# Performance work log

Measured on AMD Instinct MI355X. Metric: run time of the kernel, lower is better.

Reference implementation:

```python
import jax, jax.numpy as jnp
import numpy as np

HEAD = 16
EMB = 1024
D_K = EMB // HEAD


def setup_inputs() -> dict:
    key = jax.random.key(0)
    ks = jax.random.split(key, 11)
    B, S, E = 2, 2048, EMB
    scale = 1.0 / np.sqrt(E)
    inp = {
        "query": jax.random.normal(ks[0], (B, S, E), jnp.float32),
        "key": jax.random.normal(ks[1], (B, S, E), jnp.float32),
        "value": jax.random.normal(ks[2], (B, S, E), jnp.float32),
        "Wq": jax.random.normal(ks[3], (E, E), jnp.float32) * scale,
        "bq": jnp.zeros((E,), jnp.float32),
        "Wk": jax.random.normal(ks[4], (E, E), jnp.float32) * scale,
        "bk": jnp.zeros((E,), jnp.float32),
        "Wv": jax.random.normal(ks[5], (E, E), jnp.float32) * scale,
        "bv": jnp.zeros((E,), jnp.float32),
        "Wo": jax.random.normal(ks[6], (E, E), jnp.float32) * scale,
        "bo": jnp.zeros((E,), jnp.float32),
    }
    return inp


def reference(query, key, value, Wq, bq, Wk, bk, Wv, bv, Wo, bo):
    B, S, E = query.shape
    # 3 input projections, split into heads: [B, H, S, d_k]
    def proj(x, W, b):
        return (x @ W.T + b).reshape(B, S, HEAD, D_K).transpose(0, 2, 1, 3)

    q = proj(query, Wq, bq)
    k = proj(key, Wk, bk)
    v = proj(value, Wv, bv)

    # scaled dot-product attention (full matrix, as in original)
    scores = jnp.einsum("bhqd,bhkd->bhqk", q, k) / jnp.sqrt(jnp.float32(D_K))
    attn = jax.nn.softmax(scores, axis=-1)  # dropout in eval mode = identity
    x = jnp.einsum("bhqk,bhkd->bhqd", attn, v)

    # merge heads and output projection
    x = x.transpose(0, 2, 1, 3).reshape(B, S, E)
    return x @ Wo.T + bo
```

## Files before the change

kernel.cpp:

```cpp
#include <hip/hip_runtime.h>
#include <hip/hip_bf16.h>
#include <math.h>


constexpr int Sn = 2048;
constexpr int En = 1024;
constexpr int Hn = 16;
constexpr int Dk = 64;
constexpr int Kn = 1024;
constexpr size_t WSZ = 1048576;
constexpr size_t TSZ = 4194304;

#define QSCALE 0.18033688011112042f

typedef __bf16 bf16x8 __attribute__((ext_vector_type(8)));
typedef float  f32x4  __attribute__((ext_vector_type(4)));
typedef float  f32x16 __attribute__((ext_vector_type(16)));

union U16 { uint4 u; bf16x8 v; __hip_bfloat16 h[8]; };
union U8  { uint2 u; __hip_bfloat162 h2[2]; __hip_bfloat16 h[4]; };
union U4  { unsigned u; __hip_bfloat162 h2; };

__device__ inline U16 cvt8f(const float* __restrict__ p) {
    float4 a = *(const float4*)p;
    float4 b = *(const float4*)(p + 4);
    U16 r;
    r.h[0] = __float2bfloat16(a.x); r.h[1] = __float2bfloat16(a.y);
    r.h[2] = __float2bfloat16(a.z); r.h[3] = __float2bfloat16(a.w);
    r.h[4] = __float2bfloat16(b.x); r.h[5] = __float2bfloat16(b.y);
    r.h[6] = __float2bfloat16(b.z); r.h[7] = __float2bfloat16(b.w);
    return r;
}

__device__ inline void gload16(const __hip_bfloat16* g, __hip_bfloat16* l) {
    __builtin_amdgcn_global_load_lds(
        (const __attribute__((address_space(1))) void*)g,
        (__attribute__((address_space(3))) void*)l, 16, 0, 0);
}

template<int ROWS, int NW>
__device__ inline void stage_tile(const __hip_bfloat16* __restrict__ src, int ld,
                                  __hip_bfloat16* lds, int w, int lane) {
    int l8 = lane >> 3;
    int g = (lane & 7) ^ (l8 & 7);
    #pragma unroll
    for (int j = 0; j < ROWS / (8 * NW); ++j) {
        int c = j * NW + w;
        gload16(src + (size_t)(c * 8 + l8) * ld + g * 8, lds + c * 512);
    }
}

__global__ __launch_bounds__(256)
void cvt_w(const float* __restrict__ w0, const float* __restrict__ w1,
           const float* __restrict__ w2, const float* __restrict__ w3,
           __hip_bfloat16* __restrict__ dst)
{
    int y = blockIdx.y;
    const float* src = (y == 0) ? w0 : (y == 1) ? w1 : (y == 2) ? w2 : w3;
    size_t i = ((size_t)blockIdx.x * 256 + threadIdx.x) * 8;
    U16 r = cvt8f(src + i);
    *(uint4*)&dst[(size_t)y * WSZ + i] = r.u;
}

__global__ __launch_bounds__(256)
void cvt_x3(const float* __restrict__ q, const float* __restrict__ k,
            const float* __restrict__ v, __hip_bfloat16* __restrict__ dst)
{
    int z = blockIdx.y;
    const float* src = (z == 0) ? q : (z == 1) ? k : v;
    size_t i = ((size_t)blockIdx.x * 256 + threadIdx.x) * 8;
    U16 r = cvt8f(src + i);
    *(uint4*)&dst[(size_t)z * TSZ + i] = r.u;
}

template<int NT>
__device__ inline void gemm_core(const __hip_bfloat16* __restrict__ Ab,
                                 const __hip_bfloat16* __restrict__ Wb,
                                 __hip_bfloat16* As, __hip_bfloat16* Bs,
                                 f32x4 (&acc)[2][NT], int w, int lane)
{
    const int l15 = lane & 15, lg = lane >> 4, l7 = lane & 7;
    const int wm = (w & 1) * 32, wn = (w >> 1) * (NT * 16);
    const int coff0 = (lg ^ l7) * 8;
    const int coff1 = ((4 + lg) ^ l7) * 8;

    #pragma unroll
    for (int i = 0; i < 2; ++i)
        #pragma unroll
        for (int j = 0; j < NT; ++j) acc[i][j] = {0.f, 0.f, 0.f, 0.f};

    for (int k0 = 0; k0 < Kn; k0 += 64) {
        stage_tile<64, 4>(Ab + k0, Kn, As, w, lane);
        stage_tile<NT * 32, 4>(Wb + k0, Kn, Bs, w, lane);
        __syncthreads();

        U16 af[2][2], bf[NT][2];
        #pragma unroll
        for (int mt = 0; mt < 2; ++mt) {
            int r = (wm + mt * 16 + l15) * 64;
            af[mt][0].u = *(const uint4*)&As[r + coff0];
            af[mt][1].u = *(const uint4*)&As[r + coff1];
        }
        #pragma unroll
        for (int nt = 0; nt < NT; ++nt) {
            int r = (wn + nt * 16 + l15) * 64;
            bf[nt][0].u = *(const uint4*)&Bs[r + coff0];
            bf[nt][1].u = *(const uint4*)&Bs[r + coff1];
        }
        #pragma unroll
        for (int mt = 0; mt < 2; ++mt)
            #pragma unroll
            for (int nt = 0; nt < NT; ++nt) {
                acc[mt][nt] = __builtin_amdgcn_mfma_f32_16x16x32_bf16(af[mt][0].v, bf[nt][0].v, acc[mt][nt], 0, 0, 0);
                acc[mt][nt] = __builtin_amdgcn_mfma_f32_16x16x32_bf16(af[mt][1].v, bf[nt][1].v, acc[mt][nt], 0, 0, 0);
            }
        __syncthreads();
    }
}

__global__ __launch_bounds__(256)
void gemm_qkv(const __hip_bfloat16* __restrict__ X, const __hip_bfloat16* __restrict__ Wall,
              const float* __restrict__ bq, const float* __restrict__ bk,
              const float* __restrict__ bv, __hip_bfloat16* __restrict__ outbase)
{
    __shared__ __align__(16) __hip_bfloat16 As[64 * 64];
    __shared__ __align__(16) __hip_bfloat16 Bs[128 * 64];

    const int tid = threadIdx.x, w = tid >> 6, lane = tid & 63;
    const int z = blockIdx.z;
    const int blockM = blockIdx.x * 64, blockN = blockIdx.y * 128;

    f32x4 acc[2][4];
    gemm_core<4>(X + (size_t)z * TSZ + (size_t)blockM * Kn,
                 Wall + (size_t)z * WSZ + (size_t)blockN * Kn,
                 As, Bs, acc, w, lane);

    const float scale = (z == 0) ? QSCALE : 1.0f;
    const float* bias = (z == 0) ? bq : (z == 1) ? bk : bv;
    __hip_bfloat16* out = outbase + (size_t)z * TSZ;

    const int l15 = lane & 15, lg = lane >> 4;
    const int wm = (w & 1) * 32, wn = (w >> 1) * 64;

    #pragma unroll
    for (int nt = 0; nt < 4; ++nt) {
        int n = blockN + wn + nt * 16 + l15;
        float bvn = bias[n] * scale;
        int h_ = n >> 6, d_ = n & 63;
        #pragma unroll
        for (int mt = 0; mt < 2; ++mt) {
            int m0 = blockM + wm + mt * 16 + lg * 4;
            int b_ = m0 >> 11, s_ = m0 & (Sn - 1);
            if (z < 2) {
                #pragma unroll
                for (int i = 0; i < 4; ++i)
                    out[(((size_t)b_ * Hn + h_) * Sn + s_ + i) * Dk + d_] =
                        __float2bfloat16(fmaf(acc[mt][nt][i], scale, bvn));
            } else {
                U8 pk;
                #pragma unroll
                for (int i = 0; i < 4; ++i)
                    pk.h[i] = __float2bfloat16(fmaf(acc[mt][nt][i], scale, bvn));
                *(uint2*)&out[(((size_t)b_ * Hn + h_) * Dk + d_) * Sn + s_] = pk.u;
            }
        }
    }
}

__global__ __launch_bounds__(256)
void gemm_out(const __hip_bfloat16* __restrict__ A, const __hip_bfloat16* __restrict__ W,
              const float* __restrict__ bias, float* __restrict__ out)
{
    __shared__ __align__(16) __hip_bfloat16 As[64 * 64];
    __shared__ __align__(16) __hip_bfloat16 Bs[64 * 64];

    const int tid = threadIdx.x, w = tid >> 6, lane = tid & 63;
    const int blockM = blockIdx.x * 64, blockN = blockIdx.y * 64;

    f32x4 acc[2][2];
    gemm_core<2>(A + (size_t)blockM * Kn, W + (size_t)blockN * Kn,
                 As, Bs, acc, w, lane);

    const int l15 = lane & 15, lg = lane >> 4;
    const int wm = (w & 1) * 32, wn = (w >> 1) * 32;

    #pragma unroll
    for (int nt = 0; nt < 2; ++nt) {
        int n = blockN + wn + nt * 16 + l15;
        float bvn = bias[n];
        #pragma unroll
        for (int mt = 0; mt < 2; ++mt) {
            int m0 = blockM + wm + mt * 16 + lg * 4;
            #pragma unroll
            for (int i = 0; i < 4; ++i)
                out[(size_t)(m0 + i) * Kn + n] = acc[mt][nt][i] + bvn;
        }
    }
}

__global__ __launch_bounds__(512)
void attn(const __hip_bfloat16* __restrict__ Q, const __hip_bfloat16* __restrict__ K,
          const __hip_bfloat16* __restrict__ Vt, __hip_bfloat16* __restrict__ X)
{
    __shared__ __align__(16) __hip_bfloat16 KVs[2][2][64 * 64];
    __shared__ float Lc[4][64];

    const int bh = blockIdx.x, q0 = blockIdx.y * 128;
    const int tid = threadIdx.x, w = tid >> 6, lane = tid & 63;
    const int qs = w & 3, g = w >> 2;
    const int l31 = lane & 31, hi = lane >> 5;

    const __hip_bfloat16* Qb = Q  + (size_t)bh * Sn * Dk;
    const __hip_bfloat16* Kb = K  + (size_t)bh * Sn * Dk;
    const __hip_bfloat16* Vb = Vt + (size_t)bh * Dk * Sn;

    U16 qf[4];
    {
        const __hip_bfloat16* qp = Qb + (size_t)(q0 + qs * 32 + l31) * Dk + hi * 8;
        #pragma unroll
        for (int d0t = 0; d0t < 4; ++d0t)
            qf[d0t].u = *(const uint4*)(qp + d0t * 16);
    }

    f32x16 o[2];
    #pragma unroll
    for (int dt = 0; dt < 2; ++dt)
        #pragma unroll
        for (int r = 0; r < 16; ++r) o[dt][r] = 0.f;
    float lpart = 0.f;

    stage_tile<64, 8>(Kb, Dk, KVs[0][0], w, lane);
    stage_tile<64, 8>(Vb, Sn, KVs[0][1], w, lane);

    for (int t = 0; t < Sn / 64; ++t) {
        __syncthreads();
        const int cur = t & 1;
        if (t + 1 < Sn / 64) {
            stage_tile<64, 8>(Kb + (size_t)(t + 1) * 64 * Dk, Dk, KVs[cur ^ 1][0], w, lane);
            stage_tile<64, 8>(Vb + (t + 1) * 64, Sn, KVs[cur ^ 1][1], w, lane);
        }
        if (cur != g) continue;

        const __hip_bfloat16* Ksc = KVs[cur][0];
        const __hip_bfloat16* Vsc = KVs[cur][1];

        f32x16 st[2];
        #pragma unroll
        for (int kt = 0; kt < 2; ++kt)
            #pragma unroll
            for (int r = 0; r < 16; ++r) st[kt][r] = 0.f;

        #pragma unroll
        for (int d0t = 0; d0t < 4; ++d0t) {
            #pragma unroll
            for (int kt = 0; kt < 2; ++kt) {
                int r = kt * 32 + l31;
                int col = (((d0t * 2 + hi)) ^ (r & 7)) * 8;
                U16 kf; kf.u = *(const uint4*)&Ksc[r * 64 + col];
                st[kt] = __builtin_amdgcn_mfma_f32_32x32x16_bf16(kf.v, qf[d0t].v, st[kt], 0, 0, 0);
            }
        }

        uint4 pa[4];
        #pragma unroll
        for (int kt = 0; kt < 2; ++kt) {
            float pv[16];
            #pragma unroll
            for (int r = 0; r < 16; ++r) pv[r] = __builtin_amdgcn_exp2f(st[kt][r]);
            float s01 = (pv[0] + pv[1]) + (pv[2] + pv[3]);
            float s23 = (pv[4] + pv[5]) + (pv[6] + pv[7]);
            float s45 = (pv[8] + pv[9]) + (pv[10] + pv[11]);
            float s67 = (pv[12] + pv[13]) + (pv[14] + pv[15]);
            lpart += (s01 + s23) + (s45 + s67);

            uint wv[8];
            #pragma unroll
            for (int m2 = 0; m2 < 8; ++m2) {
                U4 pk; pk.h2 = __float22bfloat162_rn({pv[2 * m2], pv[2 * m2 + 1]});
                wv[m2] = pk.u;
            }
            asm volatile("v_permlane32_swap_b32 %0, %1" : "+v"(wv[0]), "+v"(wv[2]));
            asm volatile("v_permlane32_swap_b32 %0, %1" : "+v"(wv[1]), "+v"(wv[3]));
            asm volatile("v_permlane32_swap_b32 %0, %1" : "+v"(wv[4]), "+v"(wv[6]));
            asm volatile("v_permlane32_swap_b32 %0, %1" : "+v"(wv[5]), "+v"(wv[7]));
            pa[kt * 2 + 0] = make_uint4(wv[0], wv[1], wv[2], wv[3]);
            pa[kt * 2 + 1] = make_uint4(wv[4], wv[5], wv[6], wv[7]);
        }

        #pragma unroll
        for (int k0t = 0; k0t < 4; ++k0t) {
            U16 pau; pau.u = pa[k0t];
            #pragma unroll
            for (int dt = 0; dt < 2; ++dt) {
                int r = dt * 32 + l31;
                int col = (((k0t * 2 + hi)) ^ (r & 7)) * 8;
                U16 vf; vf.u = *(const uint4*)&Vsc[r * 64 + col];
                o[dt] = __builtin_amdgcn_mfma_f32_32x32x16_bf16(pau.v, vf.v, o[dt], 0, 0, 0);
            }
        }
    }

    __syncthreads();
    float* Ocomb = (float*)KVs;
    if (g == 0) {
        #pragma unroll
        for (int dt = 0; dt < 2; ++dt)
            #pragma unroll
            for (int r = 0; r < 16; ++r) {
                int qr = (r & 3) + 8 * (r >> 2) + 4 * hi;
                Ocomb[(qs * 32 + qr) * 64 + dt * 32 + l31] = o[dt][r];
            }
        Lc[qs][lane] = lpart;
    }
    __syncthreads();
    if (g == 1) {
        #pragma unroll
        for (int dt = 0; dt < 2; ++dt)
            #pragma unroll
            for (int r = 0; r < 16; ++r) {
                int qr = (r & 3) + 8 * (r >> 2) + 4 * hi;
                o[dt][r] += Ocomb[(qs * 32 + qr) * 64 + dt * 32 + l31];
            }
        lpart += Lc[qs][lane];
        lpart += __shfl_xor(lpart, 32, 64);
        float linv = 1.f / lpart;

        float li[16];
        #pragma unroll
        for (int r = 0; r < 16; ++r) {
            int qr = (r & 3) + 8 * (r >> 2) + 4 * hi;
            li[r] = __shfl(linv, qr, 64);
        }

        int b_ = bh >> 4, h_ = bh & (Hn - 1);
        #pragma unroll
        for (int r = 0; r < 16; ++r) {
            int qr = (r & 3) + 8 * (r >> 2) + 4 * hi;
            int sr = q0 + qs * 32 + qr;
            __hip_bfloat16* xp = X + ((size_t)(b_ * Sn + sr)) * En + h_ * Dk + l31;
            xp[0]  = __float2bfloat16(o[0][r] * li[r]);
            xp[32] = __float2bfloat16(o[1][r] * li[r]);
        }
    }
}

extern "C" void kernel_launch(void* const* d_in, const int* in_sizes, int n_in,
                              void* d_out, int out_size, void* d_ws, size_t ws_size,
                              hipStream_t stream)
{
    const float* query = (const float*)d_in[0];
    const float* key   = (const float*)d_in[1];
    const float* value = (const float*)d_in[2];
    const float* Wq = (const float*)d_in[3];
    const float* bq = (const float*)d_in[4];
    const float* Wk = (const float*)d_in[5];
    const float* bk = (const float*)d_in[6];
    const float* Wv = (const float*)d_in[7];
    const float* bv = (const float*)d_in[8];
    const float* Wo = (const float*)d_in[9];
    const float* bo = (const float*)d_in[10];
    float* out = (float*)d_out;

    __hip_bfloat16* xqkv = (__hip_bfloat16*)d_ws;
    __hip_bfloat16* Wbf  = xqkv + 3 * TSZ;
    __hip_bfloat16* QKVw = Wbf + 4 * WSZ;
    __hip_bfloat16* Xw   = xqkv;

    cvt_w<<<dim3(512, 4), 256, 0, stream>>>(Wq, Wk, Wv, Wo, Wbf);
    cvt_x3<<<dim3(2048, 3), 256, 0, stream>>>(query, key, value, xqkv);
    gemm_qkv<<<dim3(64, 8, 3), 256, 0, stream>>>(xqkv, Wbf, bq, bk, bv, QKVw);
    attn<<<dim3(32, Sn / 128), 512, 0, stream>>>(QKVw, QKVw + TSZ, QKVw + 2 * TSZ, Xw);
    gemm_out<<<dim3(64, 16), 256, 0, stream>>>(Xw, Wbf + 3 * WSZ, bo, out);
}
```

Baseline: 237.9 us.

## Split attention key tile across wave pairs and merge conversion kernels

The attention kernel moves from 512-thread blocks of 128 queries, where two wave groups alternated whole K/V tiles, to 256-thread blocks of 64 queries. In the new layout each pair of waves splits every 64-key tile into two 32-key halves, and the loop is unrolled by two so the buffer index is fixed at compile time. The goal is to keep every wave busy on each tile instead of idling half of them every iteration, and to double the grid size. This costs more redundant K/V staging per query and more block-level syncs. The weight and input fp32-to-bf16 conversion kernels are also fused into one launch to save launch overhead.

```diff
diff --git a/kernel.cpp b/kernel.cpp
--- a/kernel.cpp
+++ b/kernel.cpp
@@ -51,26 +51,29 @@
 }
 
 __global__ __launch_bounds__(256)
-void cvt_w(const float* __restrict__ w0, const float* __restrict__ w1,
-           const float* __restrict__ w2, const float* __restrict__ w3,
-           __hip_bfloat16* __restrict__ dst)
-{
-    int y = blockIdx.y;
-    const float* src = (y == 0) ? w0 : (y == 1) ? w1 : (y == 2) ? w2 : w3;
-    size_t i = ((size_t)blockIdx.x * 256 + threadIdx.x) * 8;
-    U16 r = cvt8f(src + i);
-    *(uint4*)&dst[(size_t)y * WSZ + i] = r.u;
-}
-
-__global__ __launch_bounds__(256)
-void cvt_x3(const float* __restrict__ q, const float* __restrict__ k,
-            const float* __restrict__ v, __hip_bfloat16* __restrict__ dst)
-{
-    int z = blockIdx.y;
-    const float* src = (z == 0) ? q : (z == 1) ? k : v;
-    size_t i = ((size_t)blockIdx.x * 256 + threadIdx.x) * 8;
-    U16 r = cvt8f(src + i);
-    *(uint4*)&dst[(size_t)z * TSZ + i] = r.u;
+void cvt_all(const float* __restrict__ q, const float* __restrict__ k,
+             const float* __restrict__ v,
+             const float* __restrict__ w0, const float* __restrict__ w1,
+             const float* __restrict__ w2, const float* __restrict__ w3,
+             __hip_bfloat16* __restrict__ xdst, __hip_bfloat16* __restrict__ wdst)
+{
+    int bx = blockIdx.x;
+    const float* src;
+    __hip_bfloat16* dst;
+    size_t base;
+    if (bx < 6144) {
+        int z = bx >> 11;
+        src = (z == 0) ? q : (z == 1) ? k : v;
+        dst = xdst + (size_t)z * TSZ;
+        base = ((size_t)(bx & 2047) * 256 + threadIdx.x) * 8;
+    } else {
+        int y = (bx - 6144) >> 9;
+        src = (y == 0) ? w0 : (y == 1) ? w1 : (y == 2) ? w2 : w3;
+        dst = wdst + (size_t)y * WSZ;
+        base = ((size_t)((bx - 6144) & 511) * 256 + threadIdx.x) * 8;
+    }
+    U16 r = cvt8f(src + base);
+    *(uint4*)&dst[base] = r.u;
 }
 
 template<int NT>
@@ -198,16 +201,17 @@
     }
 }
 
-__global__ __launch_bounds__(512)
+__global__ __launch_bounds__(256)
 void attn(const __hip_bfloat16* __restrict__ Q, const __hip_bfloat16* __restrict__ K,
           const __hip_bfloat16* __restrict__ Vt, __hip_bfloat16* __restrict__ X)
 {
-    __shared__ __align__(16) __hip_bfloat16 KVs[2][2][64 * 64];
-    __shared__ float Lc[4][64];
-
-    const int bh = blockIdx.x, q0 = blockIdx.y * 128;
+    __shared__ __align__(16) __hip_bfloat16 Ks[2][64 * 64];
+    __shared__ __align__(16) __hip_bfloat16 Vts[2][64 * 64];
+    __shared__ float Lc[2][64];
+
+    const int bh = blockIdx.x, q0 = blockIdx.y * 64;
     const int tid = threadIdx.x, w = tid >> 6, lane = tid & 63;
-    const int qs = w & 3, g = w >> 2;
+    const int qs = w >> 1, kh = w & 1;
     const int l31 = lane & 31, hi = lane >> 5;
 
     const __hip_bfloat16* Qb = Q  + (size_t)bh * Sn * Dk;
@@ -229,80 +233,72 @@
         for (int r = 0; r < 16; ++r) o[dt][r] = 0.f;
     float lpart = 0.f;
 
-    stage_tile<64, 8>(Kb, Dk, KVs[0][0], w, lane);
-    stage_tile<64, 8>(Vb, Sn, KVs[0][1], w, lane);
-
-    for (int t = 0; t < Sn / 64; ++t) {
+    const int rK = kh * 32 + l31;
+
+    stage_tile<64, 4>(Kb, Dk, Ks[0], w, lane);
+    stage_tile<64, 4>(Vb, Sn, Vts[0], w, lane);
+
+    auto body = [&](int cur, int tn) {
         __syncthreads();
-        const int cur = t & 1;
-        if (t + 1 < Sn / 64) {
-            stage_tile<64, 8>(Kb + (size_t)(t + 1) * 64 * Dk, Dk, KVs[cur ^ 1][0], w, lane);
-            stage_tile<64, 8>(Vb + (t + 1) * 64, Sn, KVs[cur ^ 1][1], w, lane);
-        }
-        if (cur != g) continue;
-
-        const __hip_bfloat16* Ksc = KVs[cur][0];
-        const __hip_bfloat16* Vsc = KVs[cur][1];
-
-        f32x16 st[2];
-        #pragma unroll
-        for (int kt = 0; kt < 2; ++kt)
-            #pragma unroll
-            for (int r = 0; r < 16; ++r) st[kt][r] = 0.f;
-
+        if (tn < Sn / 64) {
+            stage_tile<64, 4>(Kb + (size_t)tn * 64 * Dk, Dk, Ks[cur ^ 1], w, lane);
+            stage_tile<64, 4>(Vb + tn * 64, Sn, Vts[cur ^ 1], w, lane);
+        }
+
+        f32x16 st;
+        #pragma unroll
+        for (int r = 0; r < 16; ++r) st[r] = 0.f;
         #pragma unroll
         for (int d0t = 0; d0t < 4; ++d0t) {
-            #pragma unroll
-            for (int kt = 0; kt < 2; ++kt) {
-                int r = kt * 32 + l31;
-                int col = (((d0t * 2 + hi)) ^ (r & 7)) * 8;
-                U16 kf; kf.u = *(const uint4*)&Ksc[r * 64 + col];
-                st[kt] = __builtin_amdgcn_mfma_f32_32x32x16_bf16(kf.v, qf[d0t].v, st[kt], 0, 0, 0);
-            }
-        }
-
-        uint4 pa[4];
-        #pragma unroll
-        for (int kt = 0; kt < 2; ++kt) {
-            float pv[16];
-            #pragma unroll
-            for (int r = 0; r < 16; ++r) pv[r] = __builtin_amdgcn_exp2f(st[kt][r]);
-            float s01 = (pv[0] + pv[1]) + (pv[2] + pv[3]);
-            float s23 = (pv[4] + pv[5]) + (pv[6] + pv[7]);
-            float s45 = (pv[8] + pv[9]) + (pv[10] + pv[11]);
-            float s67 = (pv[12] + pv[13]) + (pv[14] + pv[15]);
-            lpart += (s01 + s23) + (s45 + s67);
-
-            uint wv[8];
-            #pragma unroll
-            for (int m2 = 0; m2 < 8; ++m2) {
-                U4 pk; pk.h2 = __float22bfloat162_rn({pv[2 * m2], pv[2 * m2 + 1]});
-                wv[m2] = pk.u;
-            }
-            asm volatile("v_permlane32_swap_b32 %0, %1" : "+v"(wv[0]), "+v"(wv[2]));
-            asm volatile("v_permlane32_swap_b32 %0, %1" : "+v"(wv[1]), "+v"(wv[3]));
-            asm volatile("v_permlane32_swap_b32 %0, %1" : "+v"(wv[4]), "+v"(wv[6]));
-            asm volatile("v_permlane32_swap_b32 %0, %1" : "+v"(wv[5]), "+v"(wv[7]));
-            pa[kt * 2 + 0] = make_uint4(wv[0], wv[1], wv[2], wv[3]);
-            pa[kt * 2 + 1] = make_uint4(wv[4], wv[5], wv[6], wv[7]);
-        }
-
-        #pragma unroll
-        for (int k0t = 0; k0t < 4; ++k0t) {
-            U16 pau; pau.u = pa[k0t];
+            int col = ((d0t * 2 + hi) ^ (rK & 7)) * 8;
+            U16 kf; kf.u = *(const uint4*)&Ks[cur][rK * 64 + col];
+            st = __builtin_amdgcn_mfma_f32_32x32x16_bf16(kf.v, qf[d0t].v, st, 0, 0, 0);
+        }
+
+        float pv[16];
+        #pragma unroll
+        for (int r = 0; r < 16; ++r) pv[r] = __builtin_amdgcn_exp2f(st[r]);
+        float s01 = (pv[0] + pv[1]) + (pv[2] + pv[3]);
+        float s23 = (pv[4] + pv[5]) + (pv[6] + pv[7]);
+        float s45 = (pv[8] + pv[9]) + (pv[10] + pv[11]);
+        float s67 = (pv[12] + pv[13]) + (pv[14] + pv[15]);
+        lpart += (s01 + s23) + (s45 + s67);
+
+        uint wv[8];
+        #pragma unroll
+        for (int m2 = 0; m2 < 8; ++m2) {
+            U4 pk; pk.h2 = __float22bfloat162_rn({pv[2 * m2], pv[2 * m2 + 1]});
+            wv[m2] = pk.u;
+        }
+        asm volatile("v_permlane32_swap_b32 %0, %1" : "+v"(wv[0]), "+v"(wv[2]));
+        asm volatile("v_permlane32_swap_b32 %0, %1" : "+v"(wv[1]), "+v"(wv[3]));
+        asm volatile("v_permlane32_swap_b32 %0, %1" : "+v"(wv[4]), "+v"(wv[6]));
+        asm volatile("v_permlane32_swap_b32 %0, %1" : "+v"(wv[5]), "+v"(wv[7]));
+        uint4 pa0 = make_uint4(wv[0], wv[1], wv[2], wv[3]);
+        uint4 pa1 = make_uint4(wv[4], wv[5], wv[6], wv[7]);
+
+        #pragma unroll
+        for (int j = 0; j < 2; ++j) {
+            U16 pau; pau.u = (j == 0) ? pa0 : pa1;
+            int k0t = kh * 2 + j;
             #pragma unroll
             for (int dt = 0; dt < 2; ++dt) {
-                int r = dt * 32 + l31;
-                int col = (((k0t * 2 + hi)) ^ (r & 7)) * 8;
-                U16 vf; vf.u = *(const uint4*)&Vsc[r * 64 + col];
+                int rV = dt * 32 + l31;
+                int col = ((k0t * 2 + hi) ^ (rV & 7)) * 8;
+                U16 vf; vf.u = *(const uint4*)&Vts[cur][rV * 64 + col];
                 o[dt] = __builtin_amdgcn_mfma_f32_32x32x16_bf16(pau.v, vf.v, o[dt], 0, 0, 0);
             }
         }
+    };
+
+    for (int t = 0; t < Sn / 64; t += 2) {
+        body(0, t + 1);
+        body(1, t + 2);
     }
 
     __syncthreads();
-    float* Ocomb = (float*)KVs;
-    if (g == 0) {
+    float* Ocomb = (float*)Ks;
+    if (kh == 0) {
         #pragma unroll
         for (int dt = 0; dt < 2; ++dt)
             #pragma unroll
@@ -313,7 +309,7 @@
         Lc[qs][lane] = lpart;
     }
     __syncthreads();
-    if (g == 1) {
+    if (kh == 1) {
         #pragma unroll
         for (int dt = 0; dt < 2; ++dt)
             #pragma unroll
@@ -366,9 +362,8 @@
     __hip_bfloat16* QKVw = Wbf + 4 * WSZ;
     __hip_bfloat16* Xw   = xqkv;
 
-    cvt_w<<<dim3(512, 4), 256, 0, stream>>>(Wq, Wk, Wv, Wo, Wbf);
-    cvt_x3<<<dim3(2048, 3), 256, 0, stream>>>(query, key, value, xqkv);
+    cvt_all<<<8192, 256, 0, stream>>>(query, key, value, Wq, Wk, Wv, Wo, xqkv, Wbf);
     gemm_qkv<<<dim3(64, 8, 3), 256, 0, stream>>>(xqkv, Wbf, bq, bk, bv, QKVw);
-    attn<<<dim3(32, Sn / 128), 512, 0, stream>>>(QKVw, QKVw + TSZ, QKVw + 2 * TSZ, Xw);
+    attn<<<dim3(32, Sn / 64), 256, 0, stream>>>(QKVw, QKVw + TSZ, QKVw + 2 * TSZ, Xw);
     gemm_out<<<dim3(64, 16), 256, 0, stream>>>(Xw, Wbf + 3 * WSZ, bo, out);
 }
```

Result: faster. 227.8 us (-4.2%).
